# Optimization experiments

Measured on AMD Instinct MI355X. Metric: run time of the kernel, lower is better.

The kernel has to match this reference:

```python
import jax, jax.numpy as jnp
import numpy as np


def setup_inputs() -> dict:
    key = jax.random.key(0)
    ks = jax.random.split(key, 6)
    B, Tq, Tk = 4, 512, 512
    Q, K, C = 1024, 1024, 256
    query = jax.random.normal(ks[0], (B, Tq, Q), dtype=jnp.float32)
    kmat = jax.random.normal(ks[1], (B, Tk, K), dtype=jnp.float32)
    # Linear weights (torch nn.Linear stores [out, in]; we keep [in, out] for einsum)
    Wq = jax.random.normal(ks[2], (Q, C), dtype=jnp.float32) / np.sqrt(Q)
    Wk = jax.random.normal(ks[3], (K, C), dtype=jnp.float32) / np.sqrt(K)
    w_attn = jax.random.normal(ks[4], (C,), dtype=jnp.float32) / np.sqrt(C)
    b_attn = jax.random.normal(ks[5], (), dtype=jnp.float32) * 0.01
    return {"query": query, "key": kmat, "Wq": Wq, "Wk": Wk,
            "w_attn": w_attn, "b_attn": b_attn}


def reference(query, key, Wq, Wk, w_attn, b_attn):
    # Additive (Bahdanau) attention scores.
    # q2ctx: (B, Tq, C); k2ctx: (B, Tk, C)
    q2ctx = jnp.einsum('bqi,ic->bqc', query, Wq)
    k2ctx = jnp.einsum('bki,ic->bkc', key, Wk)
    # broadcast add -> (B, Tq, Tk, C), tanh, project to scalar and squeeze
    ctx = jnp.tanh(q2ctx[:, :, None, :] + k2ctx[:, None, :, :])
    scores = jnp.einsum('bqkc,c->bqk', ctx, w_attn) + b_attn
    return scores  # (B, Tq, Tk)
```

## Files before the change

kernel.cpp:

```cpp
#include <hip/hip_runtime.h>
#include <hip/hip_bf16.h>

#define M_ROWS 2048
#define KDIM   1024
#define CDIM   256
#define TQ     512
#define TK     512

#define GBM 64
#define GBN 32
#define GBK 32

#define SCALE2LOG2E 2.8853900817779268f

typedef __attribute__((ext_vector_type(8))) short short8;
typedef __attribute__((ext_vector_type(4))) float floatx4;
typedef __attribute__((ext_vector_type(2))) float f32x2;

__device__ __forceinline__ short2 cvt2(float x, float y) {
    __hip_bfloat162 h = __float22bfloat162_rn(make_float2(x, y));
    short2 r;
    __builtin_memcpy(&r, &h, sizeof(r));
    return r;
}

__device__ __forceinline__ f32x2 splat2(float x) { return (f32x2){x, x}; }

__global__ __launch_bounds__(256) void gemm_mfma_kernel(
    const float* __restrict__ Aq, const float* __restrict__ Ak,
    const float* __restrict__ Wq, const float* __restrict__ Wk,
    const float* __restrict__ w_attn,
    float* __restrict__ Eq, float* __restrict__ Ek)
{
    __shared__ short As[GBM][GBK + 8];
    __shared__ short Ws[GBN][GBK + 8];

    const int z = blockIdx.z;
    const float* A = z ? Ak : Aq;
    const float* W = z ? Wk : Wq;
    float*       E = z ? Ek : Eq;

    const int t    = threadIdx.x;
    const int lane = t & 63;
    const int wave = t >> 6;
    const int m0   = blockIdx.x * GBM;
    const int n0   = blockIdx.y * GBN;

    const int ar = t >> 2;
    const int ac = (t & 3) * 8;
    const int wr = t >> 3;
    const int wc = (t & 7) * 4;

    const int iw = wave & 1;
    const int jw = wave >> 1;
    const int li = lane & 15;
    const int qd = lane >> 4;

    floatx4 acc0 = {0.f, 0.f, 0.f, 0.f};
    floatx4 acc1 = {0.f, 0.f, 0.f, 0.f};

    float4 a0 = *(const float4*)&A[(size_t)(m0 + ar) * KDIM + ac];
    float4 a1 = *(const float4*)&A[(size_t)(m0 + ar) * KDIM + ac + 4];
    float4 w0 = *(const float4*)&W[(size_t)wr * CDIM + n0 + wc];

    for (int k0 = 0; k0 < KDIM; k0 += GBK) {
        __syncthreads();
        short2 p0 = cvt2(a0.x, a0.y), p1 = cvt2(a0.z, a0.w);
        short2 p2 = cvt2(a1.x, a1.y), p3 = cvt2(a1.z, a1.w);
        short8 av = { p0.x, p0.y, p1.x, p1.y, p2.x, p2.y, p3.x, p3.y };
        *(short8*)&As[ar][ac] = av;
        short2 u0 = cvt2(w0.x, w0.y), u1 = cvt2(w0.z, w0.w);
        Ws[wc + 0][wr] = u0.x;
        Ws[wc + 1][wr] = u0.y;
        Ws[wc + 2][wr] = u1.x;
        Ws[wc + 3][wr] = u1.y;
        __syncthreads();
        if (k0 + GBK < KDIM) {
            a0 = *(const float4*)&A[(size_t)(m0 + ar) * KDIM + k0 + GBK + ac];
            a1 = *(const float4*)&A[(size_t)(m0 + ar) * KDIM + k0 + GBK + ac + 4];
            w0 = *(const float4*)&W[(size_t)(k0 + GBK + wr) * CDIM + n0 + wc];
        }
        short8 af  = *(const short8*)&Ws[iw * 16 + li][qd * 8];
        short8 bf0 = *(const short8*)&As[jw * 32 + li][qd * 8];
        short8 bf1 = *(const short8*)&As[jw * 32 + 16 + li][qd * 8];
        acc0 = __builtin_amdgcn_mfma_f32_16x16x32_bf16(af, bf0, acc0, 0, 0, 0);
        acc1 = __builtin_amdgcn_mfma_f32_16x16x32_bf16(af, bf1, acc1, 0, 0, 0);
    }

    #pragma unroll
    for (int r = 0; r < 4; ++r) {
        const int c = n0 + iw * 16 + qd * 4 + r;
        float scale = z ? 1.0f : (-0.5f / w_attn[c]);
        float v0 = __builtin_amdgcn_exp2f(acc0[r] * SCALE2LOG2E) * scale;
        float v1 = __builtin_amdgcn_exp2f(acc1[r] * SCALE2LOG2E) * scale;
        E[(size_t)c * M_ROWS + m0 + jw * 32 + li]      = v0;
        E[(size_t)c * M_ROWS + m0 + jw * 32 + 16 + li] = v1;
    }
}

__global__ __launch_bounds__(256) void bahdanau_kernel(
    const float* __restrict__ Eqs, const float* __restrict__ Ek,
    const float* __restrict__ w_attn, const float* __restrict__ b_attn,
    float* __restrict__ out)
{
    __shared__ float qs[64][36];
    __shared__ float ks[64][36];
    __shared__ __align__(16) float sl[CDIM];
    __shared__ float partial[4];

    const int t  = threadIdx.x;
    const int b  = blockIdx.z;
    const int q0 = blockIdx.x * 32;
    const int k0 = blockIdx.y * 32;
    const int gq = b * TQ + q0;
    const int gk = b * TK + k0;
    const int tq = (t >> 4) * 2;
    const int tk = (t & 15) * 2;

    const int lr = t >> 3;
    const int lc = (t & 7) * 4;

    {
        float wv = w_attn[t];
        sl[t] = -0.5f / wv;
        float sum = wv;
        #pragma unroll
        for (int o = 32; o >= 1; o >>= 1) sum += __shfl_down(sum, o);
        if ((t & 63) == 0) partial[t >> 6] = sum;
    }

    float4 qv[2], kv[2];
    #pragma unroll
    for (int j = 0; j < 2; ++j) {
        qv[j] = *(const float4*)&Eqs[(size_t)(lr + 32 * j) * M_ROWS + gq + lc];
        kv[j] = *(const float4*)&Ek [(size_t)(lr + 32 * j) * M_ROWS + gk + lc];
    }

    f32x2 accA = {0.f, 0.f};
    f32x2 accB = {0.f, 0.f};

    for (int ch = 0; ch < 4; ++ch) {
        __syncthreads();
        #pragma unroll
        for (int j = 0; j < 2; ++j) {
            *(float4*)&qs[lr + 32 * j][lc] = qv[j];
            *(float4*)&ks[lr + 32 * j][lc] = kv[j];
        }
        __syncthreads();
        if (ch < 3) {
            const int c1 = (ch + 1) * 64;
            #pragma unroll
            for (int j = 0; j < 2; ++j) {
                qv[j] = *(const float4*)&Eqs[(size_t)(c1 + lr + 32 * j) * M_ROWS + gq + lc];
                kv[j] = *(const float4*)&Ek [(size_t)(c1 + lr + 32 * j) * M_ROWS + gk + lc];
            }
        }
        const int cb = ch * 64;
        #pragma unroll
        for (int cc = 0; cc < 64; cc += 4) {
            float4 s4 = *(const float4*)&sl[cb + cc];
            f32x2 q1 = *(const f32x2*)&qs[cc + 0][tq];
            f32x2 q2 = *(const f32x2*)&qs[cc + 1][tq];
            f32x2 q3 = *(const f32x2*)&qs[cc + 2][tq];
            f32x2 q4 = *(const f32x2*)&qs[cc + 3][tq];
            f32x2 k1 = *(const f32x2*)&ks[cc + 0][tk];
            f32x2 k2 = *(const f32x2*)&ks[cc + 1][tk];
            f32x2 k3 = *(const f32x2*)&ks[cc + 2][tk];
            f32x2 k4 = *(const f32x2*)&ks[cc + 3][tk];
            {
                f32x2 f1 = __builtin_elementwise_fma(splat2(q1.x), k1, splat2(s4.x));
                f32x2 f2 = __builtin_elementwise_fma(splat2(q2.x), k2, splat2(s4.y));
                f32x2 f3 = __builtin_elementwise_fma(splat2(q3.x), k3, splat2(s4.z));
                f32x2 f4 = __builtin_elementwise_fma(splat2(q4.x), k4, splat2(s4.w));
                f32x2 p12 = f1 * f2, p34 = f3 * f4;
                f32x2 s12 = f1 + f2, s34 = f3 + f4;
                f32x2 num = __builtin_elementwise_fma(s12, p34, s34 * p12);
                f32x2 den = p12 * p34;
                f32x2 r = {__builtin_amdgcn_rcpf(den.x), __builtin_amdgcn_rcpf(den.y)};
                accA = __builtin_elementwise_fma(num, r, accA);
            }
            {
                f32x2 f1 = __builtin_elementwise_fma(splat2(q1.y), k1, splat2(s4.x));
                f32x2 f2 = __builtin_elementwise_fma(splat2(q2.y), k2, splat2(s4.y));
                f32x2 f3 = __builtin_elementwise_fma(splat2(q3.y), k3, splat2(s4.z));
                f32x2 f4 = __builtin_elementwise_fma(splat2(q4.y), k4, splat2(s4.w));
                f32x2 p12 = f1 * f2, p34 = f3 * f4;
                f32x2 s12 = f1 + f2, s34 = f3 + f4;
                f32x2 num = __builtin_elementwise_fma(s12, p34, s34 * p12);
                f32x2 den = p12 * p34;
                f32x2 r = {__builtin_amdgcn_rcpf(den.x), __builtin_amdgcn_rcpf(den.y)};
                accB = __builtin_elementwise_fma(num, r, accB);
            }
        }
    }

    const float bias2 = *b_attn + partial[0] + partial[1] + partial[2] + partial[3];
    float* o = out + ((size_t)b * TQ + q0 + tq) * TK + k0 + tk;
    *(float2*)&o[0]  = make_float2(accA.x + bias2, accA.y + bias2);
    *(float2*)&o[TK] = make_float2(accB.x + bias2, accB.y + bias2);
}

extern "C" void kernel_launch(void* const* d_in, const int* in_sizes, int n_in,
                              void* d_out, int out_size, void* d_ws, size_t ws_size,
                              hipStream_t stream) {
    const float* query  = (const float*)d_in[0];
    const float* key    = (const float*)d_in[1];
    const float* Wq     = (const float*)d_in[2];
    const float* Wk     = (const float*)d_in[3];
    const float* w_attn = (const float*)d_in[4];
    const float* b_attn = (const float*)d_in[5];
    float* out = (float*)d_out;

    float* Eqs = (float*)d_ws;
    float* Ek  = Eqs + (size_t)CDIM * M_ROWS;

    dim3 gemm_grid(M_ROWS / GBM, CDIM / GBN, 2);
    gemm_mfma_kernel<<<gemm_grid, 256, 0, stream>>>(query, key, Wq, Wk, w_attn, Eqs, Ek);

    dim3 main_grid(TQ / 32, TK / 32, 4);
    bahdanau_kernel<<<main_grid, 256, 0, stream>>>(Eqs, Ek, w_attn, b_attn, out);
}
```

Before: 122.7 us.

## Store exp intermediates as bf16 and load GEMM A operand directly into registers

```diff
diff --git a/kernel.cpp b/kernel.cpp
--- a/kernel.cpp
+++ b/kernel.cpp
@@ -14,6 +14,7 @@
 #define SCALE2LOG2E 2.8853900817779268f
 
 typedef __attribute__((ext_vector_type(8))) short short8;
+typedef __attribute__((ext_vector_type(8))) unsigned short ushort8;
 typedef __attribute__((ext_vector_type(4))) float floatx4;
 typedef __attribute__((ext_vector_type(2))) float f32x2;
 
@@ -23,22 +24,26 @@
     __builtin_memcpy(&r, &h, sizeof(r));
     return r;
 }
-
+__device__ __forceinline__ unsigned short f2bf1(float x) {
+    return (unsigned short)cvt2(x, x).x;
+}
+__device__ __forceinline__ float bf2f(unsigned short u) {
+    return __builtin_bit_cast(float, (unsigned)u << 16);
+}
 __device__ __forceinline__ f32x2 splat2(float x) { return (f32x2){x, x}; }
 
 __global__ __launch_bounds__(256) void gemm_mfma_kernel(
     const float* __restrict__ Aq, const float* __restrict__ Ak,
     const float* __restrict__ Wq, const float* __restrict__ Wk,
     const float* __restrict__ w_attn,
-    float* __restrict__ Eq, float* __restrict__ Ek)
+    unsigned short* __restrict__ Eq, unsigned short* __restrict__ Ek)
 {
-    __shared__ short As[GBM][GBK + 8];
     __shared__ short Ws[GBN][GBK + 8];
 
     const int z = blockIdx.z;
     const float* A = z ? Ak : Aq;
     const float* W = z ? Wk : Wq;
-    float*       E = z ? Ek : Eq;
+    unsigned short* E = z ? Ek : Eq;
 
     const int t    = threadIdx.x;
     const int lane = t & 63;
@@ -46,60 +51,64 @@
     const int m0   = blockIdx.x * GBM;
     const int n0   = blockIdx.y * GBN;
 
-    const int ar = t >> 2;
-    const int ac = (t & 3) * 8;
     const int wr = t >> 3;
     const int wc = (t & 7) * 4;
-
-    const int iw = wave & 1;
-    const int jw = wave >> 1;
     const int li = lane & 15;
     const int qd = lane >> 4;
 
+    const int row = m0 + wave * 16 + li;
+    const float* Arow = A + (size_t)row * KDIM + qd * 8;
+
     floatx4 acc0 = {0.f, 0.f, 0.f, 0.f};
     floatx4 acc1 = {0.f, 0.f, 0.f, 0.f};
 
-    float4 a0 = *(const float4*)&A[(size_t)(m0 + ar) * KDIM + ac];
-    float4 a1 = *(const float4*)&A[(size_t)(m0 + ar) * KDIM + ac + 4];
-    float4 w0 = *(const float4*)&W[(size_t)wr * CDIM + n0 + wc];
-
-    for (int k0 = 0; k0 < KDIM; k0 += GBK) {
-        __syncthreads();
-        short2 p0 = cvt2(a0.x, a0.y), p1 = cvt2(a0.z, a0.w);
-        short2 p2 = cvt2(a1.x, a1.y), p3 = cvt2(a1.z, a1.w);
-        short8 av = { p0.x, p0.y, p1.x, p1.y, p2.x, p2.y, p3.x, p3.y };
-        *(short8*)&As[ar][ac] = av;
-        short2 u0 = cvt2(w0.x, w0.y), u1 = cvt2(w0.z, w0.w);
+    float4 pa0[2], pa1[2], pw[2];
+    pa0[0] = *(const float4*)&Arow[0];
+    pa1[0] = *(const float4*)&Arow[4];
+    pw[0]  = *(const float4*)&W[(size_t)wr * CDIM + n0 + wc];
+    pa0[1] = *(const float4*)&Arow[GBK];
+    pa1[1] = *(const float4*)&Arow[GBK + 4];
+    pw[1]  = *(const float4*)&W[(size_t)(GBK + wr) * CDIM + n0 + wc];
+
+    for (int it = 0; it < KDIM / GBK; ++it) {
+        const int s = it & 1;
+        __syncthreads();
+        short2 u0 = cvt2(pw[s].x, pw[s].y), u1 = cvt2(pw[s].z, pw[s].w);
         Ws[wc + 0][wr] = u0.x;
         Ws[wc + 1][wr] = u0.y;
         Ws[wc + 2][wr] = u1.x;
         Ws[wc + 3][wr] = u1.y;
-        __syncthreads();
-        if (k0 + GBK < KDIM) {
-            a0 = *(const float4*)&A[(size_t)(m0 + ar) * KDIM + k0 + GBK + ac];
-            a1 = *(const float4*)&A[(size_t)(m0 + ar) * KDIM + k0 + GBK + ac + 4];
-            w0 = *(const float4*)&W[(size_t)(k0 + GBK + wr) * CDIM + n0 + wc];
+        short2 p0 = cvt2(pa0[s].x, pa0[s].y), p1 = cvt2(pa0[s].z, pa0[s].w);
+        short2 p2 = cvt2(pa1[s].x, pa1[s].y), p3 = cvt2(pa1[s].z, pa1[s].w);
+        short8 bv = { p0.x, p0.y, p1.x, p1.y, p2.x, p2.y, p3.x, p3.y };
+        __syncthreads();
+        if (it + 2 < KDIM / GBK) {
+            const int k0 = (it + 2) * GBK;
+            pa0[s] = *(const float4*)&Arow[k0];
+            pa1[s] = *(const float4*)&Arow[k0 + 4];
+            pw[s]  = *(const float4*)&W[(size_t)(k0 + wr) * CDIM + n0 + wc];
         }
-        short8 af  = *(const short8*)&Ws[iw * 16 + li][qd * 8];
-        short8 bf0 = *(const short8*)&As[jw * 32 + li][qd * 8];
-        short8 bf1 = *(const short8*)&As[jw * 32 + 16 + li][qd * 8];
-        acc0 = __builtin_amdgcn_mfma_f32_16x16x32_bf16(af, bf0, acc0, 0, 0, 0);
-        acc1 = __builtin_amdgcn_mfma_f32_16x16x32_bf16(af, bf1, acc1, 0, 0, 0);
+        short8 af0 = *(const short8*)&Ws[li][qd * 8];
+        short8 af1 = *(const short8*)&Ws[16 + li][qd * 8];
+        acc0 = __builtin_amdgcn_mfma_f32_16x16x32_bf16(af0, bv, acc0, 0, 0, 0);
+        acc1 = __builtin_amdgcn_mfma_f32_16x16x32_bf16(af1, bv, acc1, 0, 0, 0);
     }
 
     #pragma unroll
     for (int r = 0; r < 4; ++r) {
-        const int c = n0 + iw * 16 + qd * 4 + r;
-        float scale = z ? 1.0f : (-0.5f / w_attn[c]);
-        float v0 = __builtin_amdgcn_exp2f(acc0[r] * SCALE2LOG2E) * scale;
-        float v1 = __builtin_amdgcn_exp2f(acc1[r] * SCALE2LOG2E) * scale;
-        E[(size_t)c * M_ROWS + m0 + jw * 32 + li]      = v0;
-        E[(size_t)c * M_ROWS + m0 + jw * 32 + 16 + li] = v1;
+        const int c0 = n0 + qd * 4 + r;
+        const int c1 = c0 + 16;
+        float s0 = z ? 1.0f : (-0.5f / w_attn[c0]);
+        float s1 = z ? 1.0f : (-0.5f / w_attn[c1]);
+        float v0 = __builtin_amdgcn_exp2f(acc0[r] * SCALE2LOG2E) * s0;
+        float v1 = __builtin_amdgcn_exp2f(acc1[r] * SCALE2LOG2E) * s1;
+        E[(size_t)c0 * M_ROWS + row] = f2bf1(v0);
+        E[(size_t)c1 * M_ROWS + row] = f2bf1(v1);
     }
 }
 
 __global__ __launch_bounds__(256) void bahdanau_kernel(
-    const float* __restrict__ Eqs, const float* __restrict__ Ek,
+    const unsigned short* __restrict__ Eqs, const unsigned short* __restrict__ Ek,
     const float* __restrict__ w_attn, const float* __restrict__ b_attn,
     float* __restrict__ out)
 {
@@ -117,8 +126,8 @@
     const int tq = (t >> 4) * 2;
     const int tk = (t & 15) * 2;
 
-    const int lr = t >> 3;
-    const int lc = (t & 7) * 4;
+    const int lr = t >> 2;
+    const int lc = (t & 3) * 8;
 
     {
         float wv = w_attn[t];
@@ -129,31 +138,23 @@
         if ((t & 63) == 0) partial[t >> 6] = sum;
     }
 
-    float4 qv[2], kv[2];
-    #pragma unroll
-    for (int j = 0; j < 2; ++j) {
-        qv[j] = *(const float4*)&Eqs[(size_t)(lr + 32 * j) * M_ROWS + gq + lc];
-        kv[j] = *(const float4*)&Ek [(size_t)(lr + 32 * j) * M_ROWS + gk + lc];
-    }
+    ushort8 qu = *(const ushort8*)&Eqs[(size_t)lr * M_ROWS + gq + lc];
+    ushort8 ku = *(const ushort8*)&Ek [(size_t)lr * M_ROWS + gk + lc];
 
     f32x2 accA = {0.f, 0.f};
     f32x2 accB = {0.f, 0.f};
 
     for (int ch = 0; ch < 4; ++ch) {
         __syncthreads();
-        #pragma unroll
-        for (int j = 0; j < 2; ++j) {
-            *(float4*)&qs[lr + 32 * j][lc] = qv[j];
-            *(float4*)&ks[lr + 32 * j][lc] = kv[j];
-        }
+        *(float4*)&qs[lr][lc]     = make_float4(bf2f(qu[0]), bf2f(qu[1]), bf2f(qu[2]), bf2f(qu[3]));
+        *(float4*)&qs[lr][lc + 4] = make_float4(bf2f(qu[4]), bf2f(qu[5]), bf2f(qu[6]), bf2f(qu[7]));
+        *(float4*)&ks[lr][lc]     = make_float4(bf2f(ku[0]), bf2f(ku[1]), bf2f(ku[2]), bf2f(ku[3]));
+        *(float4*)&ks[lr][lc + 4] = make_float4(bf2f(ku[4]), bf2f(ku[5]), bf2f(ku[6]), bf2f(ku[7]));
         __syncthreads();
         if (ch < 3) {
             const int c1 = (ch + 1) * 64;
-            #pragma unroll
-            for (int j = 0; j < 2; ++j) {
-                qv[j] = *(const float4*)&Eqs[(size_t)(c1 + lr + 32 * j) * M_ROWS + gq + lc];
-                kv[j] = *(const float4*)&Ek [(size_t)(c1 + lr + 32 * j) * M_ROWS + gk + lc];
-            }
+            qu = *(const ushort8*)&Eqs[(size_t)(c1 + lr) * M_ROWS + gq + lc];
+            ku = *(const ushort8*)&Ek [(size_t)(c1 + lr) * M_ROWS + gk + lc];
         }
         const int cb = ch * 64;
         #pragma unroll
@@ -211,8 +212,8 @@
     const float* b_attn = (const float*)d_in[5];
     float* out = (float*)d_out;
 
-    float* Eqs = (float*)d_ws;
-    float* Ek  = Eqs + (size_t)CDIM * M_ROWS;
+    unsigned short* Eqs = (unsigned short*)d_ws;
+    unsigned short* Ek  = Eqs + (size_t)CDIM * M_ROWS;
 
     dim3 gemm_grid(M_ROWS / GBM, CDIM / GBN, 2);
     gemm_mfma_kernel<<<gemm_grid, 256, 0, stream>>>(query, key, Wq, Wk, w_attn, Eqs, Ek);
```

After: 110.8 us, median of 2. 1.11x faster.
